# Performance work log

Hardware: AMD Instinct MI355X
Metric: run time of the kernel (lower is better)

## Reference

```python
import jax, jax.numpy as jnp
from jax import lax
import numpy as np

STATE, ACT, TGT = 115, 39, 3
DIMS = [STATE + ACT, 16, 32, 64, 128, 64, 32, 16, 8, STATE]
B, T = 2048, 128


def setup_inputs() -> dict:
    key = jax.random.key(0)
    ks = jax.random.split(key, 2 * 9 + 3)
    inp = {"u": jax.random.normal(ks[0], (B, T, STATE + ACT), jnp.float32)}
    for i in range(9):
        fi, fo = DIMS[i], DIMS[i + 1]
        s = 1.0 / np.sqrt(fi)
        inp[f"W{i}"] = jax.random.uniform(ks[2 * i + 1], (fi, fo), jnp.float32, -s, s)
        inp[f"b{i}"] = jax.random.uniform(ks[2 * i + 2], (fo,), jnp.float32, -s, s)
    s = 1.0 / np.sqrt(STATE)
    inp["Wr"] = jax.random.uniform(ks[-2], (STATE, TGT), jnp.float32, -s, s)
    inp["br"] = jax.random.uniform(ks[-1], (TGT,), jnp.float32, -s, s)
    return inp


def reference(u, W0, b0, W1, b1, W2, b2, W3, b3, W4, b4, W5, b5, W6, b6, W7, b7, W8, b8, Wr, br):
    Ws = [W0, W1, W2, W3, W4, W5, W6, W7, W8]
    bs = [b0, b1, b2, b3, b4, b5, b6, b7, b8]

    def mlp(h):
        # 8 hidden Linear+ReLU6 layers, final Linear with no activation
        for i in range(8):
            h = jnp.clip(h @ Ws[i] + bs[i], 0.0, 6.0)  # ReLU6
        return h @ Ws[8] + bs[8]

    x0 = u[:, 0, :STATE]                      # [B, S]
    acts = jnp.swapaxes(u[:, :, -ACT:], 0, 1)  # [T, B, A]

    def step(x, a):
        xn = x + mlp(jnp.concatenate([x, a], axis=1))  # residual update
        return xn, xn

    _, xs = lax.scan(step, x0, acts)          # xs: [T, B, S] = x[:,1:,:]
    x_full = jnp.concatenate([x0[None], xs], axis=0)      # [T+1, B, S]
    x_full = jnp.swapaxes(x_full, 0, 1)                   # [B, T+1, S]

    r = x_full[:, 1:, :] @ Wr + br                        # [B, T, TGT]
    reward = -jnp.sqrt(jnp.sum(r * r, axis=2, keepdims=True))  # [B, T, 1]
    return jnp.concatenate([x_full[:, :-1, :], reward], axis=2)  # [B, T, S+1]
```

## Files before the change

### kernel.cpp

```cpp
#include <hip/hip_runtime.h>
#include <math.h>


#define TSTEPS 128
#define NB     2048
#define NST    115
#define NACT   39
#define NINF   154
#define NOUTF  116
constexpr int NT   = 256;
constexpr int ROWS = 4;

template<int CTRL>
__device__ __forceinline__ float dpp_add(float x) {
  int y = __builtin_amdgcn_update_dpp(0, __float_as_int(x), CTRL, 0xF, 0xF, true);
  return x + __int_as_float(y);
}
template<int KS>
__device__ __forceinline__ float kreduce(float a) {
  if constexpr (KS >= 2)  a = dpp_add<0xB1>(a);
  if constexpr (KS >= 4)  a = dpp_add<0x4E>(a);
  if constexpr (KS >= 8)  a = dpp_add<0x141>(a);
  if constexpr (KS >= 16) a = dpp_add<0x140>(a);
  return a;
}

__device__ __forceinline__ void barrier_lds() {
  asm volatile("s_waitcnt lgkmcnt(0)\n\ts_barrier" ::: "memory");
}
__device__ __forceinline__ void wait_lds() {
  asm volatile("s_waitcnt lgkmcnt(0)" ::: "memory");
}

template<int K, int NW, int NP, int NC, int KS, int RS, int J>
__device__ __forceinline__ void wload(const float* __restrict__ Wg,
                                      const float* __restrict__ bg,
                                      float (&w)[J][NC], float (&b)[NC], int tid) {
  static_assert(NP * KS * RS == NT, "bad cfg");
  static_assert(J * KS >= K, "bad J");
  constexpr float BS = 1.0f / (float)KS;
  const int kp = tid % KS, rest = tid / KS, cg = rest % NP;
#pragma unroll
  for (int j = 0; j < J; ++j)
#pragma unroll
    for (int c = 0; c < NC; ++c) {
      const int k = kp + KS * j, n = cg + c * NP;
      w[j][c] = (k < K && n < NW) ? Wg[k * NW + n] : 0.f;
    }
#pragma unroll
  for (int c = 0; c < NC; ++c) {
    const int n = cg + c * NP;
    b[c] = (n < NW) ? bg[n] * BS : 0.f;
  }
}

template<int K, int NW, int NP, int NC, int KS, int RS, int J, bool CLIP>
__device__ __forceinline__ void lrun(const float (&w)[J][NC], const float (&b)[NC],
                                     const float* __restrict__ in,
                                     float* __restrict__ out, int tid) {
  constexpr int RPL = ROWS / RS;
  const int kp = tid % KS, rest = tid / KS, cg = rest % NP, rg = rest / NP;
  float acc[NC][RPL];
#pragma unroll
  for (int c = 0; c < NC; ++c)
#pragma unroll
    for (int r = 0; r < RPL; ++r) acc[c][r] = b[c];

#pragma unroll
  for (int j = 0; j < J; ++j) {
    const int k = kp + KS * j;
    const float* ap = in + k * ROWS + rg * RPL;
    float av[RPL];
    if constexpr (RPL == 4) {
      float4 t = *(const float4*)ap; av[0]=t.x; av[1]=t.y; av[2]=t.z; av[3]=t.w;
    } else if constexpr (RPL == 2) {
      float2 t = *(const float2*)ap; av[0]=t.x; av[1]=t.y;
    } else {
      av[0] = *ap;
    }
#pragma unroll
    for (int c = 0; c < NC; ++c)
#pragma unroll
      for (int r = 0; r < RPL; ++r) acc[c][r] += w[j][c] * av[r];
  }
#pragma unroll
  for (int c = 0; c < NC; ++c)
#pragma unroll
    for (int r = 0; r < RPL; ++r) acc[c][r] = kreduce<KS>(acc[c][r]);

  if (kp == 0) {
#pragma unroll
    for (int c = 0; c < NC; ++c) {
      const int n = cg + c * NP;
      bool ok = true;
      if constexpr (NP * NC > NW) ok = (n < NW);
      if (ok) {
        float ov[RPL];
#pragma unroll
        for (int r = 0; r < RPL; ++r) {
          float v = acc[c][r];
          if constexpr (CLIP) v = __builtin_amdgcn_fmed3f(v, 0.f, 6.f);
          ov[r] = v;
        }
        float* op = out + n * ROWS + rg * RPL;
        if constexpr (RPL == 4)      *(float4*)op = make_float4(ov[0], ov[1], ov[2], ov[3]);
        else if constexpr (RPL == 2) *(float2*)op = make_float2(ov[0], ov[1]);
        else                         *op = ov[0];
      }
    }
  }
}

__global__ __launch_bounds__(NT, 2)
void worldnet_kernel(const float* __restrict__ u,
                     const float* __restrict__ W0, const float* __restrict__ b0,
                     const float* __restrict__ W1, const float* __restrict__ b1,
                     const float* __restrict__ W2, const float* __restrict__ b2,
                     const float* __restrict__ W3, const float* __restrict__ b3,
                     const float* __restrict__ W4, const float* __restrict__ b4,
                     const float* __restrict__ W5, const float* __restrict__ b5,
                     const float* __restrict__ W6, const float* __restrict__ b6,
                     const float* __restrict__ W7, const float* __restrict__ b7,
                     const float* __restrict__ W8, const float* __restrict__ b8,
                     const float* __restrict__ Wr, const float* __restrict__ br,
                     float* __restrict__ out) {
  __shared__ __align__(16) float sIN[160 * ROWS];
  __shared__ __align__(16) float sA[128 * ROWS];
  __shared__ __align__(16) float sB[128 * ROWS];
  const int tid = threadIdx.x, wv = tid >> 6, lane = tid & 63;

  float w0[10][1], w1[2][1], w2[8][1], w3[16][2], w4[16][2],
        w5[8][1],  w6[2][1], w7[2][1], w8[8][2],  wR[8][1];
  float c0[1], c1[1], c2[1], c3[2], c4[2], c5[1], c6[1], c7[1], c8[2], cR[1];
  wload<154, 16,  16, 1, 16, 1, 10>(W0, b0, w0, c0, tid);
  wload< 16, 32,  32, 1,  8, 1,  2>(W1, b1, w1, c1, tid);
  wload< 32, 64,  64, 1,  4, 1,  8>(W2, b2, w2, c2, tid);
  wload< 64, 128, 64, 2,  4, 1, 16>(W3, b3, w3, c3, tid);
  wload<128, 64,  32, 2,  8, 1, 16>(W4, b4, w4, c4, tid);
  wload< 64, 32,  32, 1,  8, 1,  8>(W5, b5, w5, c5, tid);
  wload< 32, 16,  16, 1, 16, 1,  2>(W6, b6, w6, c6, tid);
  wload< 16,  8,   8, 1,  8, 4,  2>(W7, b7, w7, c7, tid);
  wload<  8, 115, 64, 2,  1, 4,  8>(W8, b8, w8, c8, tid);
  wload<115,  3,   4, 1, 16, 4,  8>(Wr, br, wR, cR, tid);

  const size_t row = (size_t)blockIdx.x * ROWS + wv;
  const float* urow = u + row * (size_t)(TSTEPS * NINF);
  float* orow = out + row * (size_t)(TSTEPS * NOUTF);

  float xr0 = urow[lane];
  float xr1 = (lane < NST - 64) ? urow[lane + 64] : 0.f;
  sIN[lane * ROWS + wv] = xr0;
  orow[lane] = xr0;
  if (lane < NST - 64) {
    sIN[(lane + 64) * ROWS + wv] = xr1;
    orow[lane + 64] = xr1;
  }
  if (tid < (160 - NINF) * ROWS) sIN[NINF * ROWS + tid] = 0.f;
  float a_pre = (lane < NACT) ? urow[NST + lane] : 0.f;
  wait_lds();

#pragma unroll 1
  for (int t = 0; t < TSTEPS; ++t) {
    float* ot = orow + (size_t)t * NOUTF;

    if (lane < NACT) sIN[(NST + lane) * ROWS + wv] = a_pre;
    {
      const int tn = (t < TSTEPS - 1) ? t + 1 : t;
      a_pre = (lane < NACT) ? urow[tn * NINF + NST + lane] : 0.f;
    }
    barrier_lds();

    lrun<154, 16,  16, 1, 16, 1, 10, true >(w0, c0, sIN, sA, tid); barrier_lds();
    lrun< 16, 32,  32, 1,  8, 1,  2, true >(w1, c1, sA, sB, tid); barrier_lds();
    lrun< 32, 64,  64, 1,  4, 1,  8, true >(w2, c2, sB, sA, tid); barrier_lds();
    lrun< 64, 128, 64, 2,  4, 1, 16, true >(w3, c3, sA, sB, tid); barrier_lds();
    lrun<128, 64,  32, 2,  8, 1, 16, true >(w4, c4, sB, sA, tid); barrier_lds();
    lrun< 64, 32,  32, 1,  8, 1,  8, true >(w5, c5, sA, sB, tid); barrier_lds();
    lrun< 32, 16,  16, 1, 16, 1,  2, true >(w6, c6, sB, sA, tid); barrier_lds();

    lrun< 16,  8,   8, 1,  8, 4,  2, true >(w7, c7, sA, sB, tid);
    wait_lds();

    {
      float d0 = c8[0], d1 = c8[1];
#pragma unroll
      for (int j = 0; j < 8; ++j) {
        const float hv = sB[j * ROWS + wv];
        d0 += w8[j][0] * hv;
        d1 += w8[j][1] * hv;
      }
      float xn0 = xr0 + d0;
      float xn1 = xr1 + d1;
      const int i0 = lane * ROWS + wv, i1 = (lane + 64) * ROWS + wv;
      sIN[i0] = xn0;
      if (lane < NST - 64) sIN[i1] = xn1;
      xr0 = xn0;
      if (lane < NST - 64) xr1 = xn1;
      if (t < TSTEPS - 1) {
        float* on = ot + NOUTF;
        on[lane] = xn0;
        if (lane < NST - 64) on[lane + 64] = xn1;
      }
      wait_lds();

      const int kp = lane & 15;
      float p = cR[0];
#pragma unroll
      for (int j = 0; j < 8; ++j) {
        const int k = kp + 16 * j;
        p += wR[j][0] * sIN[k * ROWS + wv];
      }
      p = kreduce<16>(p);
      float s0 = __shfl(p, 0, 64);
      float s1 = __shfl(p, 16, 64);
      float s2 = __shfl(p, 32, 64);
      if (lane == 0) ot[NST] = -sqrtf(s0 * s0 + s1 * s1 + s2 * s2);
    }
  }
}

extern "C" void kernel_launch(void* const* d_in, const int* in_sizes, int n_in,
                              void* d_out, int out_size, void* d_ws, size_t ws_size,
                              hipStream_t stream) {
  const float* u  = (const float*)d_in[0];
  const float* W0 = (const float*)d_in[1];  const float* b0 = (const float*)d_in[2];
  const float* W1 = (const float*)d_in[3];  const float* b1 = (const float*)d_in[4];
  const float* W2 = (const float*)d_in[5];  const float* b2 = (const float*)d_in[6];
  const float* W3 = (const float*)d_in[7];  const float* b3 = (const float*)d_in[8];
  const float* W4 = (const float*)d_in[9];  const float* b4 = (const float*)d_in[10];
  const float* W5 = (const float*)d_in[11]; const float* b5 = (const float*)d_in[12];
  const float* W6 = (const float*)d_in[13]; const float* b6 = (const float*)d_in[14];
  const float* W7 = (const float*)d_in[15]; const float* b7 = (const float*)d_in[16];
  const float* W8 = (const float*)d_in[17]; const float* b8 = (const float*)d_in[18];
  const float* Wr = (const float*)d_in[19]; const float* br = (const float*)d_in[20];
  float* out = (float*)d_out;
  (void)in_sizes; (void)n_in; (void)out_size; (void)d_ws; (void)ws_size;

  dim3 grid(NB / ROWS), block(NT);
  hipLaunchKernelGGL(worldnet_kernel, grid, block, 0, stream,
                     u, W0, b0, W1, b1, W2, b2, W3, b3, W4, b4,
                     W5, b5, W6, b6, W7, b7, W8, b8, Wr, br, out);
}
```

Measured before the change: 648.9 us.

## Rebalance per-layer thread mapping, use wave-local first layers, split accumulators

Changes the per-layer thread decomposition so that threads use smaller K-splits (KS) and more K elements per thread. The first two layers become row-split (RS=4), so each wave works only on its own row. That lets them synchronise with a wave-local LDS wait instead of a block barrier, and the zero-padding init is made per-wave to match. An ACCS template parameter adds multiple independent accumulators per output to break FMA dependency chains in the long-K first layers. The cost is many more weight registers per thread (e.g. 40 for layer 0, 32 for layers 3/4), which risks spills or lower occupancy under launch_bounds(256,2).

Result: no change. 655.6 us (+1.0%).

```diff
diff --git a/kernel.cpp b/kernel.cpp
--- a/kernel.cpp
+++ b/kernel.cpp
@@ -54,17 +54,21 @@
   }
 }
 
-template<int K, int NW, int NP, int NC, int KS, int RS, int J, bool CLIP>
+template<int K, int NW, int NP, int NC, int KS, int RS, int J, bool CLIP, int ACCS>
 __device__ __forceinline__ void lrun(const float (&w)[J][NC], const float (&b)[NC],
                                      const float* __restrict__ in,
                                      float* __restrict__ out, int tid) {
   constexpr int RPL = ROWS / RS;
   const int kp = tid % KS, rest = tid / KS, cg = rest % NP, rg = rest / NP;
-  float acc[NC][RPL];
+  float acc[NC][RPL][ACCS];
 #pragma unroll
   for (int c = 0; c < NC; ++c)
 #pragma unroll
-    for (int r = 0; r < RPL; ++r) acc[c][r] = b[c];
+    for (int r = 0; r < RPL; ++r) {
+      acc[c][r][0] = b[c];
+#pragma unroll
+      for (int a = 1; a < ACCS; ++a) acc[c][r][a] = 0.f;
+    }
 
 #pragma unroll
   for (int j = 0; j < J; ++j) {
@@ -81,12 +85,17 @@
 #pragma unroll
     for (int c = 0; c < NC; ++c)
 #pragma unroll
-      for (int r = 0; r < RPL; ++r) acc[c][r] += w[j][c] * av[r];
+      for (int r = 0; r < RPL; ++r) acc[c][r][j % ACCS] += w[j][c] * av[r];
   }
 #pragma unroll
   for (int c = 0; c < NC; ++c)
 #pragma unroll
-    for (int r = 0; r < RPL; ++r) acc[c][r] = kreduce<KS>(acc[c][r]);
+    for (int r = 0; r < RPL; ++r) {
+      float s = acc[c][r][0];
+#pragma unroll
+      for (int a = 1; a < ACCS; ++a) s += acc[c][r][a];
+      acc[c][r][0] = kreduce<KS>(s);
+    }
 
   if (kp == 0) {
 #pragma unroll
@@ -98,7 +107,7 @@
         float ov[RPL];
 #pragma unroll
         for (int r = 0; r < RPL; ++r) {
-          float v = acc[c][r];
+          float v = acc[c][r][0];
           if constexpr (CLIP) v = __builtin_amdgcn_fmed3f(v, 0.f, 6.f);
           ov[r] = v;
         }
@@ -129,19 +138,19 @@
   __shared__ __align__(16) float sB[128 * ROWS];
   const int tid = threadIdx.x, wv = tid >> 6, lane = tid & 63;
 
-  float w0[10][1], w1[2][1], w2[8][1], w3[16][2], w4[16][2],
-        w5[8][1],  w6[2][1], w7[2][1], w8[8][2],  wR[8][1];
-  float c0[1], c1[1], c2[1], c3[2], c4[2], c5[1], c6[1], c7[1], c8[2], cR[1];
-  wload<154, 16,  16, 1, 16, 1, 10>(W0, b0, w0, c0, tid);
-  wload< 16, 32,  32, 1,  8, 1,  2>(W1, b1, w1, c1, tid);
-  wload< 32, 64,  64, 1,  4, 1,  8>(W2, b2, w2, c2, tid);
-  wload< 64, 128, 64, 2,  4, 1, 16>(W3, b3, w3, c3, tid);
-  wload<128, 64,  32, 2,  8, 1, 16>(W4, b4, w4, c4, tid);
-  wload< 64, 32,  32, 1,  8, 1,  8>(W5, b5, w5, c5, tid);
-  wload< 32, 16,  16, 1, 16, 1,  2>(W6, b6, w6, c6, tid);
-  wload< 16,  8,   8, 1,  8, 4,  2>(W7, b7, w7, c7, tid);
-  wload<  8, 115, 64, 2,  1, 4,  8>(W8, b8, w8, c8, tid);
-  wload<115,  3,   4, 1, 16, 4,  8>(Wr, br, wR, cR, tid);
+  float w0[40][1], w1[8][1], w2[8][1], w3[32][1], w4[32][1],
+        w5[16][1], w6[4][1], w7[2][1], w8[8][2],  wR[8][1];
+  float c0[1], c1[1], c2[1], c3[1], c4[1], c5[1], c6[1], c7[1], c8[2], cR[1];
+  wload<154, 16,   16, 1,  4, 4, 40>(W0, b0, w0, c0, tid);
+  wload< 16, 32,   32, 1,  2, 4,  8>(W1, b1, w1, c1, tid);
+  wload< 32, 64,   64, 1,  4, 1,  8>(W2, b2, w2, c2, tid);
+  wload< 64, 128, 128, 1,  2, 1, 32>(W3, b3, w3, c3, tid);
+  wload<128, 64,   64, 1,  4, 1, 32>(W4, b4, w4, c4, tid);
+  wload< 64, 32,   32, 1,  4, 2, 16>(W5, b5, w5, c5, tid);
+  wload< 32, 16,   16, 1,  8, 2,  4>(W6, b6, w6, c6, tid);
+  wload< 16,  8,    8, 1,  8, 4,  2>(W7, b7, w7, c7, tid);
+  wload<  8, 115,  64, 2,  1, 4,  8>(W8, b8, w8, c8, tid);
+  wload<115,  3,    4, 1, 16, 4,  8>(Wr, br, wR, cR, tid);
 
   const size_t row = (size_t)blockIdx.x * ROWS + wv;
   const float* urow = u + row * (size_t)(TSTEPS * NINF);
@@ -155,7 +164,7 @@
     sIN[(lane + 64) * ROWS + wv] = xr1;
     orow[lane + 64] = xr1;
   }
-  if (tid < (160 - NINF) * ROWS) sIN[NINF * ROWS + tid] = 0.f;
+  if (lane < 160 - NINF) sIN[(NINF + lane) * ROWS + wv] = 0.f;
   float a_pre = (lane < NACT) ? urow[NST + lane] : 0.f;
   wait_lds();
 
@@ -168,17 +177,19 @@
       const int tn = (t < TSTEPS - 1) ? t + 1 : t;
       a_pre = (lane < NACT) ? urow[tn * NINF + NST + lane] : 0.f;
     }
+    wait_lds();
+
+    lrun<154, 16,  16, 1, 4, 4, 40, true, 4>(w0, c0, sIN, sA, tid); wait_lds();
+    lrun< 16, 32,  32, 1, 2, 4,  8, true, 2>(w1, c1, sA, sB, tid);
     barrier_lds();
 
-    lrun<154, 16,  16, 1, 16, 1, 10, true >(w0, c0, sIN, sA, tid); barrier_lds();
-    lrun< 16, 32,  32, 1,  8, 1,  2, true >(w1, c1, sA, sB, tid); barrier_lds();
-    lrun< 32, 64,  64, 1,  4, 1,  8, true >(w2, c2, sB, sA, tid); barrier_lds();
-    lrun< 64, 128, 64, 2,  4, 1, 16, true >(w3, c3, sA, sB, tid); barrier_lds();
-    lrun<128, 64,  32, 2,  8, 1, 16, true >(w4, c4, sB, sA, tid); barrier_lds();
-    lrun< 64, 32,  32, 1,  8, 1,  8, true >(w5, c5, sA, sB, tid); barrier_lds();
-    lrun< 32, 16,  16, 1, 16, 1,  2, true >(w6, c6, sB, sA, tid); barrier_lds();
-
-    lrun< 16,  8,   8, 1,  8, 4,  2, true >(w7, c7, sA, sB, tid);
+    lrun< 32, 64,   64, 1, 4, 1,  8, true, 1>(w2, c2, sB, sA, tid); barrier_lds();
+    lrun< 64, 128, 128, 1, 2, 1, 32, true, 1>(w3, c3, sA, sB, tid); barrier_lds();
+    lrun<128, 64,   64, 1, 4, 1, 32, true, 1>(w4, c4, sB, sA, tid); barrier_lds();
+    lrun< 64, 32,   32, 1, 4, 2, 16, true, 1>(w5, c5, sA, sB, tid); barrier_lds();
+    lrun< 32, 16,   16, 1, 8, 2,  4, true, 1>(w6, c6, sB, sA, tid); barrier_lds();
+
+    lrun< 16,  8,   8, 1, 8, 4,  2, true, 1>(w7, c7, sA, sB, tid);
     wait_lds();
 
     {
```
